# Kernel tuning notes

Measured on AMD Instinct MI355X. Metric: run time of the kernel, lower is better.

Reference implementation:

```python
import jax, jax.numpy as jnp
import numpy as np

N_NODES = 100000
N_EDGES = 3200000
IN_FEATS = 768
HIDDEN = 32
NUM_CLASSES = 8


def setup_inputs() -> dict:
    key = jax.random.key(0)
    ks = jax.random.split(key, 9)
    feats = jax.random.normal(ks[0], (N_NODES, IN_FEATS), dtype=jnp.float32)
    src = jax.random.randint(ks[1], (N_EDGES,), 0, N_NODES, dtype=jnp.int32)
    dst = jax.random.randint(ks[2], (N_EDGES,), 0, N_NODES, dtype=jnp.int32)
    # DGL SAGEConv params: fc_self / fc_neigh (bias=False) + separate bias
    def glorot(k, shape):
        lim = float(np.sqrt(6.0 / (shape[0] + shape[1])))
        return jax.random.uniform(k, shape, jnp.float32, -lim, lim)
    W_self1 = glorot(ks[3], (HIDDEN, IN_FEATS))
    W_neigh1 = glorot(ks[4], (HIDDEN, IN_FEATS))
    b1 = jnp.zeros((HIDDEN,), jnp.float32)
    W_self2 = glorot(ks[5], (NUM_CLASSES, HIDDEN))
    W_neigh2 = glorot(ks[6], (NUM_CLASSES, HIDDEN))
    b2 = jnp.zeros((NUM_CLASSES,), jnp.float32)
    return {"features": feats, "src": src, "dst": dst,
            "W_self1": W_self1, "W_neigh1": W_neigh1, "b1": b1,
            "W_self2": W_self2, "W_neigh2": W_neigh2, "b2": b2}


def _sage_mean_layer(x, W_self, W_neigh, b, src, dst, n_nodes):
    # DGL: lin_before_mp when in_feats > out_feats (true for both layers here)
    h = x @ W_neigh.T                      # [N, out]
    msg = h[src]                           # [E, out] gather
    agg_sum = jax.ops.segment_sum(msg, dst, num_segments=n_nodes)
    deg = jax.ops.segment_sum(jnp.ones_like(dst, dtype=x.dtype), dst,
                              num_segments=n_nodes)
    h_neigh = agg_sum / jnp.maximum(deg, 1.0)[:, None]  # zero-in-degree -> 0
    return x @ W_self.T + h_neigh + b


def reference(features, src, dst, W_self1, W_neigh1, b1, W_self2, W_neigh2, b2):
    n = features.shape[0]
    h = _sage_mean_layer(features, W_self1, W_neigh1, b1, src, dst, n)
    h = jax.nn.relu(h)
    # dropout is identity in eval mode
    out = _sage_mean_layer(h, W_self2, W_neigh2, b2, src, dst, n)
    return out
```

## Files before the change

### kernel.cpp

```cpp
#include <hip/hip_runtime.h>
#include <hip/hip_bf16.h>

#define IN_FEATS 768
#define PART_CHUNK 4096
#define SRC_BITS 17
#define SRC_MASK 0x1FFFF

typedef __attribute__((ext_vector_type(8))) short short8v;
typedef __attribute__((ext_vector_type(4))) float f32x4;

__device__ __forceinline__ unsigned short f2bf(float f) {
    union { float f; unsigned int u; } c; c.f = f;
    unsigned int r = (c.u + 0x7FFFu + ((c.u >> 16) & 1u)) >> 16;
    return (unsigned short)r;
}
__device__ __forceinline__ float bflo(unsigned int v) {
    union { unsigned int u; float f; } c; c.u = v << 16; return c.f;
}
__device__ __forceinline__ float bfhi(unsigned int v) {
    union { unsigned int u; float f; } c; c.u = v & 0xFFFF0000u; return c.f;
}
__device__ __forceinline__ short8v pack8(float4 p, float4 q) {
    short8v r;
    r[0] = (short)f2bf(p.x); r[1] = (short)f2bf(p.y);
    r[2] = (short)f2bf(p.z); r[3] = (short)f2bf(p.w);
    r[4] = (short)f2bf(q.x); r[5] = (short)f2bf(q.y);
    r[6] = (short)f2bf(q.z); r[7] = (short)f2bf(q.w);
    return r;
}

__global__ __launch_bounds__(256) void gemm1_kernel(
    const float* __restrict__ x,
    const float* __restrict__ Wn,
    const float* __restrict__ Ws,
    const float* __restrict__ b1,
    unsigned short* __restrict__ hn1b,
    float* __restrict__ hs1,
    int N)
{
    __shared__ unsigned short As[2][64][64];
    __shared__ unsigned short Bs[2][64][64];

    const int tid  = threadIdx.x;
    const int lrow = tid >> 2;
    const int lk16 = (tid & 3) * 16;
    const int row0 = blockIdx.x * 64;

    const int  grow   = row0 + lrow;
    const bool rvalid = (grow < N);
    const float* xrow = x + (size_t)(rvalid ? grow : (N - 1)) * IN_FEATS;
    const float* wrow = (lrow < 32) ? (Wn + (size_t)lrow * IN_FEATS)
                                    : (Ws + (size_t)(lrow - 32) * IN_FEATS);

    const int w    = tid >> 6;
    const int l    = tid & 63;
    const int lr16 = l & 15;
    const int lk   = (l >> 4) * 8;

    const int sws  = (lrow & 7) << 3;
    const int ra   = w * 16 + lr16;
    const int swa  = (ra & 7) << 3;

    f32x4 acc[4];
#pragma unroll
    for (int ct = 0; ct < 4; ++ct) acc[ct] = (f32x4){0.f, 0.f, 0.f, 0.f};

    float4 a0, a1, a2, a3, w0, w1, w2, w3;
    a0 = *(const float4*)(xrow + lk16 + 0);
    a1 = *(const float4*)(xrow + lk16 + 4);
    a2 = *(const float4*)(xrow + lk16 + 8);
    a3 = *(const float4*)(xrow + lk16 + 12);
    w0 = *(const float4*)(wrow + lk16 + 0);
    w1 = *(const float4*)(wrow + lk16 + 4);
    w2 = *(const float4*)(wrow + lk16 + 8);
    w3 = *(const float4*)(wrow + lk16 + 12);

    const int NSTEP = IN_FEATS / 64;
    for (int step = 0; step < NSTEP; ++step) {
        const int buf = step & 1;
        *(short8v*)&As[buf][lrow][(lk16 + 0) ^ sws] = pack8(a0, a1);
        *(short8v*)&As[buf][lrow][(lk16 + 8) ^ sws] = pack8(a2, a3);
        *(short8v*)&Bs[buf][lrow][(lk16 + 0) ^ sws] = pack8(w0, w1);
        *(short8v*)&Bs[buf][lrow][(lk16 + 8) ^ sws] = pack8(w2, w3);
        __syncthreads();

        if (step + 1 < NSTEP) {
            const int k0 = (step + 1) * 64;
            a0 = *(const float4*)(xrow + k0 + lk16 + 0);
            a1 = *(const float4*)(xrow + k0 + lk16 + 4);
            a2 = *(const float4*)(xrow + k0 + lk16 + 8);
            a3 = *(const float4*)(xrow + k0 + lk16 + 12);
            w0 = *(const float4*)(wrow + k0 + lk16 + 0);
            w1 = *(const float4*)(wrow + k0 + lk16 + 4);
            w2 = *(const float4*)(wrow + k0 + lk16 + 8);
            w3 = *(const float4*)(wrow + k0 + lk16 + 12);
        }

        short8v af0 = *(const short8v*)&As[buf][ra][(lk +  0) ^ swa];
        short8v af1 = *(const short8v*)&As[buf][ra][(lk + 32) ^ swa];
#pragma unroll
        for (int ct = 0; ct < 4; ++ct) {
            const int rb  = ct * 16 + lr16;
            const int swb = (rb & 7) << 3;
            short8v bf0 = *(const short8v*)&Bs[buf][rb][(lk +  0) ^ swb];
            acc[ct] = __builtin_amdgcn_mfma_f32_16x16x32_bf16(af0, bf0, acc[ct], 0, 0, 0);
        }
#pragma unroll
        for (int ct = 0; ct < 4; ++ct) {
            const int rb  = ct * 16 + lr16;
            const int swb = (rb & 7) << 3;
            short8v bf1 = *(const short8v*)&Bs[buf][rb][(lk + 32) ^ swb];
            acc[ct] = __builtin_amdgcn_mfma_f32_16x16x32_bf16(af1, bf1, acc[ct], 0, 0, 0);
        }
    }

    const int rbase = row0 + w * 16 + (l >> 4) * 4;
#pragma unroll
    for (int ct = 0; ct < 4; ++ct) {
        const int ncol = ct * 16 + lr16;
        if (ncol < 32) {
#pragma unroll
            for (int j = 0; j < 4; ++j) {
                const int r = rbase + j;
                if (r < N) hn1b[(size_t)r * 32 + ncol] = f2bf(acc[ct][j]);
            }
        } else {
            const int c = ncol - 32;
            const float bias = b1[c];
#pragma unroll
            for (int j = 0; j < 4; ++j) {
                const int r = rbase + j;
                if (r < N) hs1[(size_t)r * 32 + c] = acc[ct][j] + bias;
            }
        }
    }
}

__global__ __launch_bounds__(512) void init_cursor_kernel(
    int* __restrict__ bcursor, int NB, int CAP)
{
    const int t = threadIdx.x;
    if (t < NB) bcursor[t] = t * CAP;
}

__global__ __launch_bounds__(256) void partition_kernel(
    const int* __restrict__ src, const int* __restrict__ dst,
    int* __restrict__ bcursor, unsigned int* __restrict__ packed,
    int NB, int E, int CAP)
{
    __shared__ int hcnt[512];
    __shared__ int hbase[512];
    const int t = threadIdx.x;
    for (int i = t; i < NB; i += 256) hcnt[i] = 0;
    __syncthreads();

    const int start = blockIdx.x * PART_CHUNK;
    const int end   = min(start + PART_CHUNK, E);
    const int vend  = start + ((end - start) & ~3);

    for (int i = start + t * 4; i + 3 < end; i += 1024) {
        const int4 d4 = *(const int4*)&dst[i];
        atomicAdd(&hcnt[d4.x >> 8], 1);
        atomicAdd(&hcnt[d4.y >> 8], 1);
        atomicAdd(&hcnt[d4.z >> 8], 1);
        atomicAdd(&hcnt[d4.w >> 8], 1);
    }
    for (int i = vend + t; i < end; i += 256)
        atomicAdd(&hcnt[dst[i] >> 8], 1);
    __syncthreads();

    for (int i = t; i < NB; i += 256) {
        const int c = hcnt[i];
        hbase[i] = c ? atomicAdd(&bcursor[i], c) : 0;
        hcnt[i] = 0;
    }
    __syncthreads();

    for (int i = start + t * 4; i + 3 < end; i += 1024) {
        const int4 d4 = *(const int4*)&dst[i];
        const int4 s4 = *(const int4*)&src[i];
        {
            const int b = d4.x >> 8;
            const int p = hbase[b] + atomicAdd(&hcnt[b], 1);
            if (p < (b + 1) * CAP) packed[p] = ((unsigned int)(d4.x & 255) << SRC_BITS) | (unsigned int)s4.x;
        }
        {
            const int b = d4.y >> 8;
            const int p = hbase[b] + atomicAdd(&hcnt[b], 1);
            if (p < (b + 1) * CAP) packed[p] = ((unsigned int)(d4.y & 255) << SRC_BITS) | (unsigned int)s4.y;
        }
        {
            const int b = d4.z >> 8;
            const int p = hbase[b] + atomicAdd(&hcnt[b], 1);
            if (p < (b + 1) * CAP) packed[p] = ((unsigned int)(d4.z & 255) << SRC_BITS) | (unsigned int)s4.z;
        }
        {
            const int b = d4.w >> 8;
            const int p = hbase[b] + atomicAdd(&hcnt[b], 1);
            if (p < (b + 1) * CAP) packed[p] = ((unsigned int)(d4.w & 255) << SRC_BITS) | (unsigned int)s4.w;
        }
    }
    for (int i = vend + t; i < end; i += 256) {
        const int d = dst[i];
        const int b = d >> 8;
        const int p = hbase[b] + atomicAdd(&hcnt[b], 1);
        if (p < (b + 1) * CAP) packed[p] = ((unsigned int)(d & 255) << SRC_BITS) | (unsigned int)src[i];
    }
}

__global__ __launch_bounds__(1024) void csr_finalize_kernel(
    const unsigned int* __restrict__ packed, const int* __restrict__ bcursor,
    int* __restrict__ rowstart, int* __restrict__ rowcnt,
    int* __restrict__ edge_src, int N, int CAP)
{
    __shared__ int cnt[256];
    __shared__ int sdata[256];
    __shared__ int cur[256];
    const int b = blockIdx.x;
    const int t = threadIdx.x;
    const int base = b * CAP;
    const int endp = min(bcursor[b], base + CAP);

    if (t < 256) cnt[t] = 0;
    __syncthreads();
    for (int i = base + t; i < endp; i += 1024)
        atomicAdd(&cnt[packed[i] >> SRC_BITS], 1);
    __syncthreads();

    if (t < 256) sdata[t] = cnt[t];
    __syncthreads();
    for (int off = 1; off < 256; off <<= 1) {
        const int add = (t < 256 && t >= off) ? sdata[t - off] : 0;
        __syncthreads();
        if (t < 256) sdata[t] += add;
        __syncthreads();
    }
    if (t < 256) {
        const int excl = (t > 0) ? sdata[t - 1] : 0;
        const int n = (b << 8) + t;
        if (n < N) {
            rowstart[n] = base + excl;
            rowcnt[n]   = cnt[t];
        }
        cur[t] = base + excl;
    }
    __syncthreads();

    for (int i = base + t; i < endp; i += 1024) {
        const unsigned int v = packed[i];
        const int pos = atomicAdd(&cur[v >> SRC_BITS], 1);
        edge_src[pos] = (int)(v & SRC_MASK);
    }
}

__global__ __launch_bounds__(256) void agg1_fused_kernel(
    const unsigned short* __restrict__ hn1b, const float* __restrict__ hs1,
    const int* __restrict__ rowstart, const int* __restrict__ rowcnt,
    const int* __restrict__ edge_src,
    const float* __restrict__ Wn2, const float* __restrict__ Ws2,
    const float* __restrict__ b2,
    unsigned short* __restrict__ hn2b, float* __restrict__ hs2, int N)
{
    __shared__ float w2[16][33];
    __shared__ float bb[8];
    __shared__ float hsm[16][33];

    const int tid = threadIdx.x;
    const int g   = tid >> 4;
    const int ln  = tid & 15;

    w2[tid >> 5][tid & 31]       = Wn2[tid];
    w2[8 + (tid >> 5)][tid & 31] = Ws2[tid];
    if (tid < 8) bb[tid] = b2[tid];

    const unsigned int* hn1u = (const unsigned int*)hn1b;

    const int n = blockIdx.x * 16 + g;
    float sx = 0.f, sy = 0.f;
    int degi = 0;
    if (n < N) {
        const int rs = rowstart[n];
        degi = rowcnt[n];
        const int re = rs + degi;
        int e = rs;
        for (; e + 8 <= re; e += 8) {
            const int s0 = edge_src[e + 0];
            const int s1 = edge_src[e + 1];
            const int s2 = edge_src[e + 2];
            const int s3 = edge_src[e + 3];
            const int s4 = edge_src[e + 4];
            const int s5 = edge_src[e + 5];
            const int s6 = edge_src[e + 6];
            const int s7 = edge_src[e + 7];
            const unsigned int v0 = hn1u[(size_t)s0 * 16 + ln];
            const unsigned int v1 = hn1u[(size_t)s1 * 16 + ln];
            const unsigned int v2 = hn1u[(size_t)s2 * 16 + ln];
            const unsigned int v3 = hn1u[(size_t)s3 * 16 + ln];
            const unsigned int v4 = hn1u[(size_t)s4 * 16 + ln];
            const unsigned int v5 = hn1u[(size_t)s5 * 16 + ln];
            const unsigned int v6 = hn1u[(size_t)s6 * 16 + ln];
            const unsigned int v7 = hn1u[(size_t)s7 * 16 + ln];
            sx += ((bflo(v0) + bflo(v1)) + (bflo(v2) + bflo(v3)))
                + ((bflo(v4) + bflo(v5)) + (bflo(v6) + bflo(v7)));
            sy += ((bfhi(v0) + bfhi(v1)) + (bfhi(v2) + bfhi(v3)))
                + ((bfhi(v4) + bfhi(v5)) + (bfhi(v6) + bfhi(v7)));
        }
        for (; e < re; ++e) {
            const unsigned int v = hn1u[(size_t)edge_src[e] * 16 + ln];
            sx += bflo(v); sy += bfhi(v);
        }
        const float inv = 1.0f / fmaxf((float)degi, 1.0f);
        const float2 hs = *(const float2*)(hs1 + (size_t)n * 32 + 2 * ln);
        hsm[g][2 * ln + 0] = fmaxf(hs.x + sx * inv, 0.0f);
        hsm[g][2 * ln + 1] = fmaxf(hs.y + sy * inv, 0.0f);
    }
    __syncthreads();

    if (n < N) {
        const float* wrow = w2[ln];
        const float* hv   = hsm[g];
        float acc = 0.0f;
#pragma unroll
        for (int k = 0; k < 32; ++k) acc += wrow[k] * hv[k];
        if (ln < 8) hn2b[(size_t)n * 8 + ln] = f2bf(acc);
        else        hs2[(size_t)n * 8 + (ln - 8)] = acc + bb[ln - 8];
    }
}

__global__ __launch_bounds__(256) void agg2_fused_kernel(
    const unsigned short* __restrict__ hn2b, const float* __restrict__ hs2,
    const int* __restrict__ rowstart, const int* __restrict__ rowcnt,
    const int* __restrict__ edge_src,
    float* __restrict__ out, int N)
{
    const int tid  = threadIdx.x;
    const int g    = tid >> 4;
    const int ln   = tid & 15;
    const int slot = ln >> 2;
    const int q    = ln & 3;

    const unsigned int* hn2u = (const unsigned int*)hn2b;

    const int n = blockIdx.x * 16 + g;
    float sx = 0.f, sy = 0.f;
    int degi = 0;
    if (n < N) {
        const int rs = rowstart[n];
        degi = rowcnt[n];
        const int re = rs + degi;
        for (int e = rs + slot; e < re; e += 4) {
            const unsigned int v = hn2u[(size_t)edge_src[e] * 4 + q];
            sx += bflo(v); sy += bfhi(v);
        }
    }
    sx += __shfl_xor(sx, 4, 64);  sy += __shfl_xor(sy, 4, 64);
    sx += __shfl_xor(sx, 8, 64);  sy += __shfl_xor(sy, 8, 64);

    if (n < N && slot == 0) {
        const float inv = 1.0f / fmaxf((float)degi, 1.0f);
        const float2 s = *(const float2*)(hs2 + (size_t)n * 8 + 2 * q);
        float2 o;
        o.x = s.x + sx * inv;
        o.y = s.y + sy * inv;
        *(float2*)(out + (size_t)n * 8 + 2 * q) = o;
    }
}

extern "C" void kernel_launch(void* const* d_in, const int* in_sizes, int n_in,
                              void* d_out, int out_size, void* d_ws, size_t ws_size,
                              hipStream_t stream)
{
    const float* feats = (const float*)d_in[0];
    const int*   src   = (const int*)d_in[1];
    const int*   dst   = (const int*)d_in[2];
    const float* Ws1   = (const float*)d_in[3];
    const float* Wn1   = (const float*)d_in[4];
    const float* b1    = (const float*)d_in[5];
    const float* Ws2   = (const float*)d_in[6];
    const float* Wn2   = (const float*)d_in[7];
    const float* b2    = (const float*)d_in[8];
    float* out = (float*)d_out;

    const int N  = in_sizes[0] / IN_FEATS;
    const int E  = in_sizes[1];
    const int NB = (N + 255) >> 8;
    const int CAP = (int)((((2LL * E) / NB) + 255) & ~255LL);

    char* ws = (char*)d_ws;
    const size_t N32 = (size_t)N * 32;
    const size_t N8  = (size_t)N * 8;
    unsigned short* hn1b = (unsigned short*)ws;
    ws += ((N32 * 2 + 255) / 256) * 256;
    float* hs1 = (float*)ws;
    ws += ((N32 * 4 + 255) / 256) * 256;
    unsigned short* hn2b = (unsigned short*)ws;
    ws += ((N8 * 2 + 255) / 256) * 256;
    float* hs2 = (float*)ws;
    ws += ((N8 * 4 + 255) / 256) * 256;
    int* rowstart = (int*)ws;
    ws += (((size_t)N * 4 + 255) / 256) * 256;
    int* rowcnt = (int*)ws;
    ws += (((size_t)N * 4 + 255) / 256) * 256;
    int* bcursor = (int*)ws;
    ws += 512 * 4;
    unsigned int* packed = (unsigned int*)ws;
    ws += (((size_t)NB * CAP * 4 + 255) / 256) * 256;
    int* edge_src = (int*)ws;

    const int nbPart = (E + PART_CHUNK - 1) / PART_CHUNK;

    init_cursor_kernel<<<1, 512, 0, stream>>>(bcursor, NB, CAP);
    partition_kernel<<<nbPart, 256, 0, stream>>>(src, dst, bcursor, packed,
                                                 NB, E, CAP);
    csr_finalize_kernel<<<NB, 1024, 0, stream>>>(packed, bcursor, rowstart,
                                                 rowcnt, edge_src, N, CAP);

    gemm1_kernel<<<(N + 63) / 64, 256, 0, stream>>>(feats, Wn1, Ws1, b1,
                                                    hn1b, hs1, N);

    agg1_fused_kernel<<<(N + 15) / 16, 256, 0, stream>>>(
        hn1b, hs1, rowstart, rowcnt, edge_src, Wn2, Ws2, b2, hn2b, hs2, N);

    agg2_fused_kernel<<<(N + 15) / 16, 256, 0, stream>>>(
        hn2b, hs2, rowstart, rowcnt, edge_src, out, N);
}
```

Measured before the change: 255.6 us.

## Fuse edge partition with GEMM1 and split hidden features into halves

```diff
diff --git a/kernel.cpp b/kernel.cpp
--- a/kernel.cpp
+++ b/kernel.cpp
@@ -2,7 +2,7 @@
 #include <hip/hip_bf16.h>
 
 #define IN_FEATS 768
-#define PART_CHUNK 4096
+#define PART_CHUNK 8192
 #define SRC_BITS 17
 #define SRC_MASK 0x1FFFF
 
@@ -29,22 +29,98 @@
     return r;
 }
 
-__global__ __launch_bounds__(256) void gemm1_kernel(
+__global__ __launch_bounds__(512) void init_cursor_kernel(
+    int* __restrict__ bcursor, int NB, int CAP)
+{
+    const int t = threadIdx.x;
+    if (t < NB) bcursor[t] = t * CAP;
+}
+
+__global__ __launch_bounds__(256) void gemm_part_kernel(
     const float* __restrict__ x,
     const float* __restrict__ Wn,
     const float* __restrict__ Ws,
     const float* __restrict__ b1,
     unsigned short* __restrict__ hn1b,
     float* __restrict__ hs1,
-    int N)
-{
-    __shared__ unsigned short As[2][64][64];
-    __shared__ unsigned short Bs[2][64][64];
-
-    const int tid  = threadIdx.x;
+    int N,
+    const int* __restrict__ src, const int* __restrict__ dst,
+    int* __restrict__ bcursor, unsigned int* __restrict__ packed,
+    int NB, int E, int CAP, int nbPart)
+{
+    __shared__ __align__(16) unsigned char smem[36864];
+    const int tid = threadIdx.x;
+
+    if ((int)blockIdx.x < nbPart) {
+        int* hcnt  = (int*)smem;
+        int* hbase = hcnt + 512;
+
+        for (int i = tid; i < NB; i += 256) hcnt[i] = 0;
+        __syncthreads();
+
+        const int start = blockIdx.x * PART_CHUNK;
+        const int end   = min(start + PART_CHUNK, E);
+        const int vend  = start + ((end - start) & ~3);
+
+        for (int i = start + tid * 4; i + 3 < end; i += 1024) {
+            const int4 d4 = *(const int4*)&dst[i];
+            atomicAdd(&hcnt[d4.x >> 8], 1);
+            atomicAdd(&hcnt[d4.y >> 8], 1);
+            atomicAdd(&hcnt[d4.z >> 8], 1);
+            atomicAdd(&hcnt[d4.w >> 8], 1);
+        }
+        for (int i = vend + tid; i < end; i += 256)
+            atomicAdd(&hcnt[dst[i] >> 8], 1);
+        __syncthreads();
+
+        for (int i = tid; i < NB; i += 256) {
+            const int c = hcnt[i];
+            hbase[i] = c ? atomicAdd(&bcursor[i], c) : 0;
+            hcnt[i] = 0;
+        }
+        __syncthreads();
+
+        for (int i = start + tid * 4; i + 3 < end; i += 1024) {
+            const int4 d4 = *(const int4*)&dst[i];
+            const int4 s4 = *(const int4*)&src[i];
+            {
+                const int b = d4.x >> 8;
+                const int p = hbase[b] + atomicAdd(&hcnt[b], 1);
+                if (p < (b + 1) * CAP) packed[p] = ((unsigned int)(d4.x & 255) << SRC_BITS) | (unsigned int)s4.x;
+            }
+            {
+                const int b = d4.y >> 8;
+                const int p = hbase[b] + atomicAdd(&hcnt[b], 1);
+                if (p < (b + 1) * CAP) packed[p] = ((unsigned int)(d4.y & 255) << SRC_BITS) | (unsigned int)s4.y;
+            }
+            {
+                const int b = d4.z >> 8;
+                const int p = hbase[b] + atomicAdd(&hcnt[b], 1);
+                if (p < (b + 1) * CAP) packed[p] = ((unsigned int)(d4.z & 255) << SRC_BITS) | (unsigned int)s4.z;
+            }
+            {
+                const int b = d4.w >> 8;
+                const int p = hbase[b] + atomicAdd(&hcnt[b], 1);
+                if (p < (b + 1) * CAP) packed[p] = ((unsigned int)(d4.w & 255) << SRC_BITS) | (unsigned int)s4.w;
+            }
+        }
+        for (int i = vend + tid; i < end; i += 256) {
+            const int d = dst[i];
+            const int b = d >> 8;
+            const int p = hbase[b] + atomicAdd(&hcnt[b], 1);
+            if (p < (b + 1) * CAP) packed[p] = ((unsigned int)(d & 255) << SRC_BITS) | (unsigned int)src[i];
+        }
+        return;
+    }
+
+    unsigned short* AsB = (unsigned short*)smem;
+    unsigned short* BsB = AsB + 2 * 64 * 72;
+#define AS(b, r) (AsB + ((b) * 64 + (r)) * 72)
+#define BS(b, r) (BsB + ((b) * 64 + (r)) * 72)
+
     const int lrow = tid >> 2;
     const int lk16 = (tid & 3) * 16;
-    const int row0 = blockIdx.x * 64;
+    const int row0 = ((int)blockIdx.x - nbPart) * 64;
 
     const int  grow   = row0 + lrow;
     const bool rvalid = (grow < N);
@@ -56,10 +132,6 @@
     const int l    = tid & 63;
     const int lr16 = l & 15;
     const int lk   = (l >> 4) * 8;
-
-    const int sws  = (lrow & 7) << 3;
-    const int ra   = w * 16 + lr16;
-    const int swa  = (ra & 7) << 3;
 
     f32x4 acc[4];
 #pragma unroll
@@ -78,10 +150,10 @@
     const int NSTEP = IN_FEATS / 64;
     for (int step = 0; step < NSTEP; ++step) {
         const int buf = step & 1;
-        *(short8v*)&As[buf][lrow][(lk16 + 0) ^ sws] = pack8(a0, a1);
-        *(short8v*)&As[buf][lrow][(lk16 + 8) ^ sws] = pack8(a2, a3);
-        *(short8v*)&Bs[buf][lrow][(lk16 + 0) ^ sws] = pack8(w0, w1);
-        *(short8v*)&Bs[buf][lrow][(lk16 + 8) ^ sws] = pack8(w2, w3);
+        *(short8v*)(AS(buf, lrow) + lk16)     = pack8(a0, a1);
+        *(short8v*)(AS(buf, lrow) + lk16 + 8) = pack8(a2, a3);
+        *(short8v*)(BS(buf, lrow) + lk16)     = pack8(w0, w1);
+        *(short8v*)(BS(buf, lrow) + lk16 + 8) = pack8(w2, w3);
         __syncthreads();
 
         if (step + 1 < NSTEP) {
@@ -96,33 +168,34 @@
             w3 = *(const float4*)(wrow + k0 + lk16 + 12);
         }
 
-        short8v af0 = *(const short8v*)&As[buf][ra][(lk +  0) ^ swa];
-        short8v af1 = *(const short8v*)&As[buf][ra][(lk + 32) ^ swa];
+        short8v af0 = *(const short8v*)(AS(buf, w * 16 + lr16) + lk);
+        short8v af1 = *(const short8v*)(AS(buf, w * 16 + lr16) + lk + 32);
 #pragma unroll
         for (int ct = 0; ct < 4; ++ct) {
-            const int rb  = ct * 16 + lr16;
-            const int swb = (rb & 7) << 3;
-            short8v bf0 = *(const short8v*)&Bs[buf][rb][(lk +  0) ^ swb];
+            short8v bf0 = *(const short8v*)(BS(buf, ct * 16 + lr16) + lk);
             acc[ct] = __builtin_amdgcn_mfma_f32_16x16x32_bf16(af0, bf0, acc[ct], 0, 0, 0);
         }
 #pragma unroll
         for (int ct = 0; ct < 4; ++ct) {
-            const int rb  = ct * 16 + lr16;
-            const int swb = (rb & 7) << 3;
-            short8v bf1 = *(const short8v*)&Bs[buf][rb][(lk + 32) ^ swb];
+            short8v bf1 = *(const short8v*)(BS(buf, ct * 16 + lr16) + lk + 32);
             acc[ct] = __builtin_amdgcn_mfma_f32_16x16x32_bf16(af1, bf1, acc[ct], 0, 0, 0);
         }
     }
+#undef AS
+#undef BS
 
     const int rbase = row0 + w * 16 + (l >> 4) * 4;
 #pragma unroll
     for (int ct = 0; ct < 4; ++ct) {
         const int ncol = ct * 16 + lr16;
         if (ncol < 32) {
+            const int half = ncol >> 4;
+            const int c16  = ncol & 15;
+            unsigned short* hd = hn1b + (size_t)half * N * 16;
 #pragma unroll
             for (int j = 0; j < 4; ++j) {
                 const int r = rbase + j;
-                if (r < N) hn1b[(size_t)r * 32 + ncol] = f2bf(acc[ct][j]);
+                if (r < N) hd[(size_t)r * 16 + c16] = f2bf(acc[ct][j]);
             }
         } else {
             const int c = ncol - 32;
@@ -133,78 +206,6 @@
                 if (r < N) hs1[(size_t)r * 32 + c] = acc[ct][j] + bias;
             }
         }
-    }
-}
-
-__global__ __launch_bounds__(512) void init_cursor_kernel(
-    int* __restrict__ bcursor, int NB, int CAP)
-{
-    const int t = threadIdx.x;
-    if (t < NB) bcursor[t] = t * CAP;
-}
-
-__global__ __launch_bounds__(256) void partition_kernel(
-    const int* __restrict__ src, const int* __restrict__ dst,
-    int* __restrict__ bcursor, unsigned int* __restrict__ packed,
-    int NB, int E, int CAP)
-{
-    __shared__ int hcnt[512];
-    __shared__ int hbase[512];
-    const int t = threadIdx.x;
-    for (int i = t; i < NB; i += 256) hcnt[i] = 0;
-    __syncthreads();
-
-    const int start = blockIdx.x * PART_CHUNK;
-    const int end   = min(start + PART_CHUNK, E);
-    const int vend  = start + ((end - start) & ~3);
-
-    for (int i = start + t * 4; i + 3 < end; i += 1024) {
-        const int4 d4 = *(const int4*)&dst[i];
-        atomicAdd(&hcnt[d4.x >> 8], 1);
-        atomicAdd(&hcnt[d4.y >> 8], 1);
-        atomicAdd(&hcnt[d4.z >> 8], 1);
-        atomicAdd(&hcnt[d4.w >> 8], 1);
-    }
-    for (int i = vend + t; i < end; i += 256)
-        atomicAdd(&hcnt[dst[i] >> 8], 1);
-    __syncthreads();
-
-    for (int i = t; i < NB; i += 256) {
-        const int c = hcnt[i];
-        hbase[i] = c ? atomicAdd(&bcursor[i], c) : 0;
-        hcnt[i] = 0;
-    }
-    __syncthreads();
-
-    for (int i = start + t * 4; i + 3 < end; i += 1024) {
-        const int4 d4 = *(const int4*)&dst[i];
-        const int4 s4 = *(const int4*)&src[i];
-        {
-            const int b = d4.x >> 8;
-            const int p = hbase[b] + atomicAdd(&hcnt[b], 1);
-            if (p < (b + 1) * CAP) packed[p] = ((unsigned int)(d4.x & 255) << SRC_BITS) | (unsigned int)s4.x;
-        }
-        {
-            const int b = d4.y >> 8;
-            const int p = hbase[b] + atomicAdd(&hcnt[b], 1);
-            if (p < (b + 1) * CAP) packed[p] = ((unsigned int)(d4.y & 255) << SRC_BITS) | (unsigned int)s4.y;
-        }
-        {
-            const int b = d4.z >> 8;
-            const int p = hbase[b] + atomicAdd(&hcnt[b], 1);
-            if (p < (b + 1) * CAP) packed[p] = ((unsigned int)(d4.z & 255) << SRC_BITS) | (unsigned int)s4.z;
-        }
-        {
-            const int b = d4.w >> 8;
-            const int p = hbase[b] + atomicAdd(&hcnt[b], 1);
-            if (p < (b + 1) * CAP) packed[p] = ((unsigned int)(d4.w & 255) << SRC_BITS) | (unsigned int)s4.w;
-        }
-    }
-    for (int i = vend + t; i < end; i += 256) {
-        const int d = dst[i];
-        const int b = d >> 8;
-        const int p = hbase[b] + atomicAdd(&hcnt[b], 1);
-        if (p < (b + 1) * CAP) packed[p] = ((unsigned int)(d & 255) << SRC_BITS) | (unsigned int)src[i];
     }
 }
 
@@ -254,7 +255,8 @@
 }
 
 __global__ __launch_bounds__(256) void agg1_fused_kernel(
-    const unsigned short* __restrict__ hn1b, const float* __restrict__ hs1,
+    const unsigned short* __restrict__ hn1b,
+    const float* __restrict__ hs1,
     const int* __restrict__ rowstart, const int* __restrict__ rowcnt,
     const int* __restrict__ edge_src,
     const float* __restrict__ Wn2, const float* __restrict__ Ws2,
@@ -263,67 +265,64 @@
 {
     __shared__ float w2[16][33];
     __shared__ float bb[8];
-    __shared__ float hsm[16][33];
+    __shared__ float hsm[32][33];
 
     const int tid = threadIdx.x;
-    const int g   = tid >> 4;
-    const int ln  = tid & 15;
+    const int g   = tid >> 3;
+    const int ln  = tid & 7;
 
     w2[tid >> 5][tid & 31]       = Wn2[tid];
     w2[8 + (tid >> 5)][tid & 31] = Ws2[tid];
     if (tid < 8) bb[tid] = b2[tid];
 
-    const unsigned int* hn1u = (const unsigned int*)hn1b;
-
-    const int n = blockIdx.x * 16 + g;
-    float sx = 0.f, sy = 0.f;
-    int degi = 0;
+    const int n = blockIdx.x * 32 + g;
+    int rs = 0, degi = 0;
+    if (n < N) { rs = rowstart[n]; degi = rowcnt[n]; }
+    const float inv = 1.0f / fmaxf((float)degi, 1.0f);
+    const int re = rs + degi;
+
+#pragma unroll
+    for (int h = 0; h < 2; ++h) {
+        const unsigned int* tab = (const unsigned int*)hn1b + (size_t)h * N * 8;
+        float sx = 0.f, sy = 0.f;
+        if (n < N) {
+            int e = rs;
+            for (; e + 4 <= re; e += 4) {
+                const int s0 = edge_src[e + 0];
+                const int s1 = edge_src[e + 1];
+                const int s2 = edge_src[e + 2];
+                const int s3 = edge_src[e + 3];
+                const unsigned int v0 = tab[(size_t)s0 * 8 + ln];
+                const unsigned int v1 = tab[(size_t)s1 * 8 + ln];
+                const unsigned int v2 = tab[(size_t)s2 * 8 + ln];
+                const unsigned int v3 = tab[(size_t)s3 * 8 + ln];
+                sx += (bflo(v0) + bflo(v1)) + (bflo(v2) + bflo(v3));
+                sy += (bfhi(v0) + bfhi(v1)) + (bfhi(v2) + bfhi(v3));
+            }
+            for (; e < re; ++e) {
+                const unsigned int v = tab[(size_t)edge_src[e] * 8 + ln];
+                sx += bflo(v); sy += bfhi(v);
+            }
+            const int f = h * 16 + 2 * ln;
+            const float2 hsv = *(const float2*)(hs1 + (size_t)n * 32 + f);
+            hsm[g][f + 0] = fmaxf(hsv.x + sx * inv, 0.0f);
+            hsm[g][f + 1] = fmaxf(hsv.y + sy * inv, 0.0f);
+        }
+    }
+    __syncthreads();
+
     if (n < N) {
-        const int rs = rowstart[n];
-        degi = rowcnt[n];
-        const int re = rs + degi;
-        int e = rs;
-        for (; e + 8 <= re; e += 8) {
-            const int s0 = edge_src[e + 0];
-            const int s1 = edge_src[e + 1];
-            const int s2 = edge_src[e + 2];
-            const int s3 = edge_src[e + 3];
-            const int s4 = edge_src[e + 4];
-            const int s5 = edge_src[e + 5];
-            const int s6 = edge_src[e + 6];
-            const int s7 = edge_src[e + 7];
-            const unsigned int v0 = hn1u[(size_t)s0 * 16 + ln];
-            const unsigned int v1 = hn1u[(size_t)s1 * 16 + ln];
-            const unsigned int v2 = hn1u[(size_t)s2 * 16 + ln];
-            const unsigned int v3 = hn1u[(size_t)s3 * 16 + ln];
-            const unsigned int v4 = hn1u[(size_t)s4 * 16 + ln];
-            const unsigned int v5 = hn1u[(size_t)s5 * 16 + ln];
-            const unsigned int v6 = hn1u[(size_t)s6 * 16 + ln];
-            const unsigned int v7 = hn1u[(size_t)s7 * 16 + ln];
-            sx += ((bflo(v0) + bflo(v1)) + (bflo(v2) + bflo(v3)))
-                + ((bflo(v4) + bflo(v5)) + (bflo(v6) + bflo(v7)));
-            sy += ((bfhi(v0) + bfhi(v1)) + (bfhi(v2) + bfhi(v3)))
-                + ((bfhi(v4) + bfhi(v5)) + (bfhi(v6) + bfhi(v7)));
-        }
-        for (; e < re; ++e) {
-            const unsigned int v = hn1u[(size_t)edge_src[e] * 16 + ln];
-            sx += bflo(v); sy += bfhi(v);
-        }
-        const float inv = 1.0f / fmaxf((float)degi, 1.0f);
-        const float2 hs = *(const float2*)(hs1 + (size_t)n * 32 + 2 * ln);
-        hsm[g][2 * ln + 0] = fmaxf(hs.x + sx * inv, 0.0f);
-        hsm[g][2 * ln + 1] = fmaxf(hs.y + sy * inv, 0.0f);
-    }
-    __syncthreads();
-
-    if (n < N) {
-        const float* wrow = w2[ln];
-        const float* hv   = hsm[g];
-        float acc = 0.0f;
-#pragma unroll
-        for (int k = 0; k < 32; ++k) acc += wrow[k] * hv[k];
-        if (ln < 8) hn2b[(size_t)n * 8 + ln] = f2bf(acc);
-        else        hs2[(size_t)n * 8 + (ln - 8)] = acc + bb[ln - 8];
+        const float* hv = hsm[g];
+#pragma unroll
+        for (int o2 = 0; o2 < 2; ++o2) {
+            const int o = o2 * 8 + ln;
+            const float* wr = w2[o];
+            float acc = 0.0f;
+#pragma unroll
+            for (int k = 0; k < 32; ++k) acc += wr[k] * hv[k];
+            if (o < 8) hn2b[(size_t)n * 8 + o] = f2bf(acc);
+            else       hs2[(size_t)n * 8 + (o - 8)] = acc + bb[o - 8];
+        }
     }
 }
 
@@ -408,17 +407,18 @@
     int* edge_src = (int*)ws;
 
     const int nbPart = (E + PART_CHUNK - 1) / PART_CHUNK;
+    const int nbGemm = (N + 63) / 64;
 
     init_cursor_kernel<<<1, 512, 0, stream>>>(bcursor, NB, CAP);
-    partition_kernel<<<nbPart, 256, 0, stream>>>(src, dst, bcursor, packed,
-                                                 NB, E, CAP);
+
+    gemm_part_kernel<<<nbPart + nbGemm, 256, 0, stream>>>(
+        feats, Wn1, Ws1, b1, hn1b, hs1, N,
+        src, dst, bcursor, packed, NB, E, CAP, nbPart);
+
     csr_finalize_kernel<<<NB, 1024, 0, stream>>>(packed, bcursor, rowstart,
                                                  rowcnt, edge_src, N, CAP);
 
-    gemm1_kernel<<<(N + 63) / 64, 256, 0, stream>>>(feats, Wn1, Ws1, b1,
-                                                    hn1b, hs1, N);
-
-    agg1_fused_kernel<<<(N + 15) / 16, 256, 0, stream>>>(
+    agg1_fused_kernel<<<(N + 31) / 32, 256, 0, stream>>>(
         hn1b, hs1, rowstart, rowcnt, edge_src, Wn2, Ws2, b2, hn2b, hs2, N);
 
     agg2_fused_kernel<<<(N + 15) / 16, 256, 0, stream>>>(
```

Result: faster. 239.3 us (median of 2 runs) (-6.4%).
